# Kernel tuning notes

Hardware: AMD Instinct MI355X
Metric: run time of the kernel (lower is better)

The kernel has to match this reference:

```python
import jax, jax.numpy as jnp
import numpy as np

N, E, D_IN, D_H = 20000, 320000, 512, 512
ALPHA = 0.1
LAMBDA = 1.0

def setup_inputs() -> dict:
    key = jax.random.key(0)
    ks = jax.random.split(key, 12)
    feat = jax.random.normal(ks[0], (N, D_IN), dtype=jnp.float32)
    src = jax.random.randint(ks[1], (E,), 0, N, dtype=jnp.int32)
    dst = jax.random.randint(ks[2], (E,), 0, N, dtype=jnp.int32)
    s = 0.05
    fc_w = jax.random.normal(ks[3], (D_H, D_IN), dtype=jnp.float32) * s  # torch Linear: [out,in]
    fc_b = jax.random.normal(ks[4], (D_H,), dtype=jnp.float32) * s
    w1_1 = jax.random.normal(ks[5], (D_H, D_H), dtype=jnp.float32) * s
    w2_1 = jax.random.normal(ks[6], (D_H, D_H), dtype=jnp.float32) * s
    b_1 = jax.random.normal(ks[7], (D_H,), dtype=jnp.float32) * s
    w1_2 = jax.random.normal(ks[8], (D_H, D_H), dtype=jnp.float32) * s
    w2_2 = jax.random.normal(ks[9], (D_H, D_H), dtype=jnp.float32) * s
    b_2 = jax.random.normal(ks[10], (D_H,), dtype=jnp.float32) * s
    return {"feat": feat, "src": src, "dst": dst, "fc_w": fc_w, "fc_b": fc_b,
            "w1_1": w1_1, "w2_1": w2_1, "b_1": b_1,
            "w1_2": w1_2, "w2_2": w2_2, "b_2": b_2}


def _gcn2_layer(h, h0, src, dst, norm, w1, w2, b, layer):
    # DGL GCN2Conv (project_initial_features=False)
    beta = float(np.log(LAMBDA / layer + 1.0))
    x = h * norm                      # [N, D]
    agg = jax.ops.segment_sum(x[src], dst, num_segments=h.shape[0])  # SpMM: sum over in-neighbors
    agg = agg * norm
    f = agg * (1.0 - ALPHA)
    f0 = h0 * ALPHA
    rst = ((1.0 - beta) * f + beta * (f @ w1)
           + (1.0 - beta) * f0 + beta * (f0 @ w2) + b)
    return jax.nn.relu(rst)


def reference(feat, src, dst, fc_w, fc_b, w1_1, w2_1, b_1, w1_2, w2_2, b_2):
    n = feat.shape[0]
    h = feat @ fc_w.T + fc_b          # initial projection
    # symmetric norm from in-degrees (clamped at 1), as in DGL
    deg = jax.ops.segment_sum(jnp.ones_like(dst, dtype=h.dtype), dst, num_segments=n)
    norm = jnp.clip(deg, 1.0, None) ** -0.5
    norm = norm[:, None]
    res = _gcn2_layer(h, h, src, dst, norm, w1_1, w2_1, b_1, layer=1)
    out = _gcn2_layer(res, h, src, dst, norm, w1_2, w2_2, b_2, layer=2)
    return out
```

## Files before the change

kernel.cpp:

```cpp
#include <hip/hip_runtime.h>
#include <hip/hip_bf16.h>
#include <stdint.h>
#include <stddef.h>

typedef __bf16 bf16_t;
typedef __bf16 bf16x4 __attribute__((ext_vector_type(4)));
typedef __bf16 bf16x8 __attribute__((ext_vector_type(8)));
typedef float floatx4 __attribute__((ext_vector_type(4)));

#define NN 20000
#define EE 320000
#define DD 512
#define CAP 96
#define BETA1 0.6931471805599453f
#define BETA2 0.40546510810816444f

__device__ __forceinline__ void gload16(const bf16_t* g, bf16_t* l) {
  __builtin_amdgcn_global_load_lds((const __attribute__((address_space(1))) uint32_t*)g,
                                   (__attribute__((address_space(3))) uint32_t*)l, 16, 0, 0);
}

__global__ void bucket_kernel(const int* __restrict__ src, const int* __restrict__ dst,
                              int* __restrict__ cnt, int* __restrict__ esrc, int E) {
  int e = blockIdx.x * 256 + threadIdx.x;
  if (e < E) {
    int d = dst[e];
    int pos = atomicAdd(&cnt[d], 1);
    if (pos < CAP) esrc[d * CAP + pos] = src[e];
  }
}

__global__ void norm_kernel(const int* __restrict__ cnt, float* __restrict__ nrm, int n) {
  int i = blockIdx.x * 256 + threadIdx.x;
  if (i < n) nrm[i] = 1.0f / sqrtf(fmaxf((float)cnt[i], 1.0f));
}

__global__ void cvt_kernel(const float* __restrict__ in, bf16_t* __restrict__ out, int n4) {
  int i = blockIdx.x * 256 + threadIdx.x;
  if (i < n4) {
    float4 v = ((const float4*)in)[i];
    bf16x4 o = {(bf16_t)v.x, (bf16_t)v.y, (bf16_t)v.z, (bf16_t)v.w};
    ((bf16x4*)out)[i] = o;
  }
}

__global__ void transpose_cat(const float* __restrict__ W1, const float* __restrict__ W2,
                              bf16_t* __restrict__ BT, int K) {
  __shared__ bf16_t tile[32][33];
  int k0 = blockIdx.y * 32;
  int n0 = blockIdx.x * 32;
  int tx = threadIdx.x, ty = threadIdx.y;
  const float* W = (k0 < 512) ? W1 : W2;
  int kk = (k0 < 512) ? k0 : (k0 - 512);
#pragma unroll
  for (int i = 0; i < 32; i += 8)
    tile[ty + i][tx] = (bf16_t)W[(size_t)(kk + ty + i) * 512 + n0 + tx];
  __syncthreads();
#pragma unroll
  for (int i = 0; i < 32; i += 8)
    BT[(size_t)(n0 + ty + i) * K + k0 + tx] = tile[tx][ty + i];
}

__global__ __launch_bounds__(256) void aggregate_kernel(
    const bf16_t* __restrict__ hin, const float* __restrict__ nrm,
    const int* __restrict__ cnt, const int* __restrict__ esrc,
    bf16_t* __restrict__ Acat) {
  int node = blockIdx.x * 4 + (threadIdx.x >> 6);
  if (node >= NN) return;
  int lane = threadIdx.x & 63;
  const int* eb = esrc + (size_t)node * CAP;
  int n_e = cnt[node];
  n_e = n_e < CAP ? n_e : CAP;

  float acc[8] = {};
  bf16x8 v0 = {}, v1 = {}, v2 = {}, v3 = {}, v4 = {}, v5 = {}, v6 = {}, v7 = {};
  float ns0 = 0, ns1 = 0, ns2 = 0, ns3 = 0, ns4 = 0, ns5 = 0, ns6 = 0, ns7 = 0;

#define LOADJ(j, idx)                                                  \
  {                                                                    \
    int s = eb[idx];                                                   \
    ns##j = nrm[s];                                                    \
    v##j = *(const bf16x8*)(hin + (size_t)s * DD + lane * 8);          \
  }
#define SLOT(j, i)                                                     \
  if ((i) + (j) < n_e) {                                               \
    bf16x8 a = v##j; float na = ns##j;                                 \
    if ((i) + (j) + 8 < n_e) LOADJ(j, (i) + (j) + 8)                   \
    _Pragma("unroll")                                                  \
    for (int k = 0; k < 8; ++k) acc[k] += na * (float)a[k];            \
  }

  if (0 < n_e) LOADJ(0, 0)
  if (1 < n_e) LOADJ(1, 1)
  if (2 < n_e) LOADJ(2, 2)
  if (3 < n_e) LOADJ(3, 3)
  if (4 < n_e) LOADJ(4, 4)
  if (5 < n_e) LOADJ(5, 5)
  if (6 < n_e) LOADJ(6, 6)
  if (7 < n_e) LOADJ(7, 7)

  for (int i = 0; i < n_e; i += 8) {
    SLOT(0, i)
    SLOT(1, i)
    SLOT(2, i)
    SLOT(3, i)
    SLOT(4, i)
    SLOT(5, i)
    SLOT(6, i)
    SLOT(7, i)
  }
#undef SLOT
#undef LOADJ

  float nd = 0.9f * nrm[node];
  bf16x8 ob;
#pragma unroll
  for (int k = 0; k < 8; ++k) ob[k] = (bf16_t)(nd * acc[k]);
  *(bf16x8*)(Acat + (size_t)node * 1024 + lane * 8) = ob;
}

template <int MODE>
__global__ __launch_bounds__(256) void gemm_kernel(
    const bf16_t* __restrict__ A, const bf16_t* __restrict__ BT,
    int lda, int ldb, int K, int M,
    const float* __restrict__ bias,
    const bf16_t* __restrict__ acat_ro, float beta,
    float* __restrict__ outf, bf16_t* __restrict__ outb,
    bf16_t* __restrict__ acat2) {
  __shared__ bf16_t As[2][64 * 64];
  __shared__ bf16_t Bs[2][128 * 64];

  const int bid = blockIdx.x;
  const int mt = (bid >> 5) * 8 + (bid & 7);
  const int nt = (bid >> 3) & 3;
  const int m0 = mt * 64;
  if (m0 >= M) return;
  const int n0 = nt * 128;

  const int t = threadIdx.x;
  const int lane = t & 63;
  const int w = t >> 6;
  const int wm = w & 1, wn = w >> 1;
  const int quad = lane >> 4, m16 = lane & 15;

  const int tr = t >> 3;
  const int gc = (t & 7) ^ (tr & 7);
  int arow0 = m0 + tr;      arow0 = arow0 < M ? arow0 : M - 1;
  int arow1 = m0 + tr + 32; arow1 = arow1 < M ? arow1 : M - 1;
  const bf16_t* agp0 = A + (size_t)arow0 * lda + gc * 8;
  const bf16_t* agp1 = A + (size_t)arow1 * lda + gc * 8;
  const bf16_t* bgp0 = BT + (size_t)(n0 + tr) * ldb + gc * 8;
  const bf16_t* bgp1 = BT + (size_t)(n0 + tr + 32) * ldb + gc * 8;
  const bf16_t* bgp2 = BT + (size_t)(n0 + tr + 64) * ldb + gc * 8;
  const bf16_t* bgp3 = BT + (size_t)(n0 + tr + 96) * ldb + gc * 8;

#define STAGE(buf, ko)                              \
  gload16(agp0 + (ko), &As[buf][t * 8]);            \
  gload16(agp1 + (ko), &As[buf][(t + 256) * 8]);    \
  gload16(bgp0 + (ko), &Bs[buf][t * 8]);            \
  gload16(bgp1 + (ko), &Bs[buf][(t + 256) * 8]);    \
  gload16(bgp2 + (ko), &Bs[buf][(t + 512) * 8]);    \
  gload16(bgp3 + (ko), &Bs[buf][(t + 768) * 8]);

  floatx4 acc[2][4] = {};
  const int niter = K >> 6;

  STAGE(0, 0)

  for (int kt = 0; kt < niter; ++kt) {
    __syncthreads();
    const int b = kt & 1;
    if (kt + 1 < niter) {
      const int ko = (kt + 1) * 64;
      STAGE(b ^ 1, ko)
    }

#pragma unroll
    for (int ks = 0; ks < 2; ++ks) {
      bf16x8 af[2], bfr[4];
#pragma unroll
      for (int i = 0; i < 2; ++i) {
        int arow = wm * 32 + i * 16 + m16;
        int cc = (ks * 4 + quad) ^ (arow & 7);
        af[i] = *(const bf16x8*)(&As[b][(arow * 8 + cc) * 8]);
      }
#pragma unroll
      for (int j = 0; j < 4; ++j) {
        int brow = wn * 64 + j * 16 + m16;
        int cc = (ks * 4 + quad) ^ (brow & 7);
        bfr[j] = *(const bf16x8*)(&Bs[b][(brow * 8 + cc) * 8]);
      }
#pragma unroll
      for (int i = 0; i < 2; ++i)
#pragma unroll
        for (int j = 0; j < 4; ++j)
          acc[i][j] = __builtin_amdgcn_mfma_f32_16x16x32_bf16(af[i], bfr[j], acc[i][j], 0, 0, 0);
    }
  }
#undef STAGE

#pragma unroll
  for (int i = 0; i < 2; ++i) {
#pragma unroll
    for (int j = 0; j < 4; ++j) {
      int col = n0 + wn * 64 + j * 16 + m16;
      float bv = bias[col];
#pragma unroll
      for (int p = 0; p < 4; ++p) {
        int row = m0 + wm * 32 + i * 16 + quad * 4 + p;
        if (row < M) {
          size_t idx = (size_t)row * DD + col;
          float v = acc[i][j][p];
          if constexpr (MODE == 0) {
            float hv = v + bv;
            outb[idx] = (bf16_t)hv;
            acat2[(size_t)row * 1024 + 512 + col] = (bf16_t)(0.1f * hv);
          } else {
            float fsv = (float)acat_ro[(size_t)row * 1024 + col] +
                        (float)acat_ro[(size_t)row * 1024 + 512 + col];
            float r = (1.0f - beta) * fsv + beta * v + bv;
            r = fmaxf(r, 0.0f);
            if constexpr (MODE == 1) outb[idx] = (bf16_t)r;
            else outf[idx] = r;
          }
        }
      }
    }
  }
}

extern "C" void kernel_launch(void* const* d_in, const int* in_sizes, int n_in,
                              void* d_out, int out_size, void* d_ws, size_t ws_size,
                              hipStream_t stream) {
  const float* feat = (const float*)d_in[0];
  const int* src = (const int*)d_in[1];
  const int* dst = (const int*)d_in[2];
  const float* fc_w = (const float*)d_in[3];
  const float* fc_b = (const float*)d_in[4];
  const float* w1_1 = (const float*)d_in[5];
  const float* w2_1 = (const float*)d_in[6];
  const float* b_1  = (const float*)d_in[7];
  const float* w1_2 = (const float*)d_in[8];
  const float* w2_2 = (const float*)d_in[9];
  const float* b_2  = (const float*)d_in[10];
  float* out = (float*)d_out;

  char* ws = (char*)d_ws;
  size_t off = 0;
  auto alloc = [&](size_t bytes) {
    char* p = ws + off;
    off += (bytes + 255) & ~(size_t)255;
    return p;
  };
  const size_t NDf = (size_t)NN * DD;
  bf16_t* h_bf   = (bf16_t*)alloc(NDf * sizeof(bf16_t));
  bf16_t* res_bf = (bf16_t*)alloc(NDf * sizeof(bf16_t));
  bf16_t* featb  = (bf16_t*)alloc(NDf * sizeof(bf16_t));
  bf16_t* Acat   = (bf16_t*)alloc((size_t)NN * 1024 * sizeof(bf16_t));
  bf16_t* BW0    = (bf16_t*)alloc((size_t)512 * 512 * sizeof(bf16_t));
  bf16_t* BT1    = (bf16_t*)alloc((size_t)512 * 1024 * sizeof(bf16_t));
  bf16_t* BT2    = (bf16_t*)alloc((size_t)512 * 1024 * sizeof(bf16_t));
  int*    cnt    = (int*)alloc((size_t)NN * sizeof(int));
  float*  nrm    = (float*)alloc((size_t)NN * sizeof(float));
  int*    esrc   = (int*)alloc((size_t)NN * CAP * sizeof(int));

  hipMemsetAsync(cnt, 0, (size_t)NN * sizeof(int), stream);
  bucket_kernel<<<(EE + 255) / 256, 256, 0, stream>>>(src, dst, cnt, esrc, EE);
  norm_kernel<<<(NN + 255) / 256, 256, 0, stream>>>(cnt, nrm, NN);

  cvt_kernel<<<(int)(NDf / 4 / 256), 256, 0, stream>>>(feat, featb, (int)(NDf / 4));
  cvt_kernel<<<(512 * 512 / 4) / 256, 256, 0, stream>>>(fc_w, BW0, 512 * 512 / 4);

  transpose_cat<<<dim3(16, 32), dim3(32, 8), 0, stream>>>(w1_1, w2_1, BT1, 1024);
  transpose_cat<<<dim3(16, 32), dim3(32, 8), 0, stream>>>(w1_2, w2_2, BT2, 1024);

  const int gblocks = 1280;

  gemm_kernel<0><<<gblocks, 256, 0, stream>>>(featb, BW0, 512, 512, 512, NN, fc_b,
                                              nullptr, 0.0f, nullptr, h_bf, Acat);

  aggregate_kernel<<<(NN + 3) / 4, 256, 0, stream>>>(h_bf, nrm, cnt, esrc, Acat);
  gemm_kernel<1><<<gblocks, 256, 0, stream>>>(Acat, BT1, 1024, 1024, 1024, NN, b_1,
                                              Acat, BETA1, nullptr, res_bf, nullptr);

  aggregate_kernel<<<(NN + 3) / 4, 256, 0, stream>>>(res_bf, nrm, cnt, esrc, Acat);
  gemm_kernel<2><<<gblocks, 256, 0, stream>>>(Acat, BT2, 1024, 1024, 1024, NN, b_2,
                                              Acat, BETA2, out, nullptr, nullptr);
}
```

Measured before the change: 363.1 us.

## Triple-buffer GEMM LDS staging with explicit vmcnt waits

Moves the GEMM main loop from double to triple buffering in LDS. Tiles are prefetched two iterations ahead, and the loop waits with s_waitcnt vmcnt(6) so the newest stage's loads can stay in flight while the current tile is computed. The goal is to hide more global-load latency behind the MFMA work. In exchange, LDS per block grows from 48KB to 72KB, which may cut occupancy, and the hand-written waitcnt and barrier code depends on the exact count of outstanding loads to stay correct.

```diff
diff --git a/kernel.cpp b/kernel.cpp
--- a/kernel.cpp
+++ b/kernel.cpp
@@ -127,8 +127,8 @@
     const bf16_t* __restrict__ acat_ro, float beta,
     float* __restrict__ outf, bf16_t* __restrict__ outb,
     bf16_t* __restrict__ acat2) {
-  __shared__ bf16_t As[2][64 * 64];
-  __shared__ bf16_t Bs[2][128 * 64];
+  __shared__ bf16_t As[3][64 * 64];
+  __shared__ bf16_t Bs[3][128 * 64];
 
   const int bid = blockIdx.x;
   const int mt = (bid >> 5) * 8 + (bid & 7);
@@ -162,42 +162,58 @@
   gload16(bgp2 + (ko), &Bs[buf][(t + 512) * 8]);    \
   gload16(bgp3 + (ko), &Bs[buf][(t + 768) * 8]);
 
+#define COMPUTE(b)                                                               \
+  _Pragma("unroll")                                                              \
+  for (int ks = 0; ks < 2; ++ks) {                                               \
+    bf16x8 af[2], bfr[4];                                                        \
+    _Pragma("unroll")                                                            \
+    for (int i = 0; i < 2; ++i) {                                                \
+      int arow = wm * 32 + i * 16 + m16;                                         \
+      int cc = (ks * 4 + quad) ^ (arow & 7);                                     \
+      af[i] = *(const bf16x8*)(&As[b][(arow * 8 + cc) * 8]);                     \
+    }                                                                            \
+    _Pragma("unroll")                                                            \
+    for (int j = 0; j < 4; ++j) {                                                \
+      int brow = wn * 64 + j * 16 + m16;                                         \
+      int cc = (ks * 4 + quad) ^ (brow & 7);                                     \
+      bfr[j] = *(const bf16x8*)(&Bs[b][(brow * 8 + cc) * 8]);                    \
+    }                                                                            \
+    _Pragma("unroll")                                                            \
+    for (int i = 0; i < 2; ++i)                                                  \
+      _Pragma("unroll")                                                          \
+      for (int j = 0; j < 4; ++j)                                                \
+        acc[i][j] = __builtin_amdgcn_mfma_f32_16x16x32_bf16(af[i], bfr[j],       \
+                                                            acc[i][j], 0, 0, 0); \
+  }
+
   floatx4 acc[2][4] = {};
   const int niter = K >> 6;
 
   STAGE(0, 0)
-
-  for (int kt = 0; kt < niter; ++kt) {
-    __syncthreads();
-    const int b = kt & 1;
-    if (kt + 1 < niter) {
-      const int ko = (kt + 1) * 64;
-      STAGE(b ^ 1, ko)
+  STAGE(1, 64)
+
+  int cur = 0;
+  for (int kt = 0; kt < niter - 1; ++kt) {
+    asm volatile("s_waitcnt vmcnt(6)" ::: "memory");
+    asm volatile("s_waitcnt lgkmcnt(0)" ::: "memory");
+    __builtin_amdgcn_s_barrier();
+    __builtin_amdgcn_sched_barrier(0);
+    if (kt + 2 < niter) {
+      int nxt = cur + 2; nxt = nxt >= 3 ? nxt - 3 : nxt;
+      const int ko = (kt + 2) * 64;
+      STAGE(nxt, ko)
     }
-
-#pragma unroll
-    for (int ks = 0; ks < 2; ++ks) {
-      bf16x8 af[2], bfr[4];
-#pragma unroll
-      for (int i = 0; i < 2; ++i) {
-        int arow = wm * 32 + i * 16 + m16;
-        int cc = (ks * 4 + quad) ^ (arow & 7);
-        af[i] = *(const bf16x8*)(&As[b][(arow * 8 + cc) * 8]);
-      }
-#pragma unroll
-      for (int j = 0; j < 4; ++j) {
-        int brow = wn * 64 + j * 16 + m16;
-        int cc = (ks * 4 + quad) ^ (brow & 7);
-        bfr[j] = *(const bf16x8*)(&Bs[b][(brow * 8 + cc) * 8]);
-      }
-#pragma unroll
-      for (int i = 0; i < 2; ++i)
-#pragma unroll
-        for (int j = 0; j < 4; ++j)
-          acc[i][j] = __builtin_amdgcn_mfma_f32_16x16x32_bf16(af[i], bfr[j], acc[i][j], 0, 0, 0);
-    }
-  }
+    COMPUTE(cur)
+    cur = (cur == 2) ? 0 : cur + 1;
+  }
+  asm volatile("s_waitcnt vmcnt(0)" ::: "memory");
+  asm volatile("s_waitcnt lgkmcnt(0)" ::: "memory");
+  __builtin_amdgcn_s_barrier();
+  __builtin_amdgcn_sched_barrier(0);
+  COMPUTE(cur)
+
 #undef STAGE
+#undef COMPUTE
 
 #pragma unroll
   for (int i = 0; i < 2; ++i) {
```

After: 382.7 us. 1.05x slower.

## Pre-tile GEMM operands into MFMA fragment layout and drop LDS staging

Applied to the files above, without the earlier changes.

Operands (features, weights, and the aggregated Acat buffer) are now written in a blocked layout that matches the MFMA fragment order. This lets the GEMM load fragments straight from global memory with no LDS double buffering and no barriers. The conversion, transpose and count-zeroing kernels are merged into one prep kernel, and the norm kernel is removed by computing rsqrt of the degree inline in aggregation. The risk is that each wave reads its fragments from global memory independently, with no sharing through LDS across the block, so L2 traffic and latency exposure may rise.

```diff
diff --git a/kernel.cpp b/kernel.cpp
--- a/kernel.cpp
+++ b/kernel.cpp
@@ -12,16 +12,14 @@
 #define EE 320000
 #define DD 512
 #define CAP 96
+#define NBLK 313
 #define BETA1 0.6931471805599453f
 #define BETA2 0.40546510810816444f
 
-__device__ __forceinline__ void gload16(const bf16_t* g, bf16_t* l) {
-  __builtin_amdgcn_global_load_lds((const __attribute__((address_space(1))) uint32_t*)g,
-                                   (__attribute__((address_space(3))) uint32_t*)l, 16, 0, 0);
-}
-
-__global__ void bucket_kernel(const int* __restrict__ src, const int* __restrict__ dst,
-                              int* __restrict__ cnt, int* __restrict__ esrc, int E) {
+
+__global__ __launch_bounds__(256) void bucket_kernel(
+    const int* __restrict__ src, const int* __restrict__ dst,
+    int* __restrict__ cnt, int* __restrict__ esrc, int E) {
   int e = blockIdx.x * 256 + threadIdx.x;
   if (e < E) {
     int d = dst[e];
@@ -30,47 +28,64 @@
   }
 }
 
-__global__ void norm_kernel(const int* __restrict__ cnt, float* __restrict__ nrm, int n) {
-  int i = blockIdx.x * 256 + threadIdx.x;
-  if (i < n) nrm[i] = 1.0f / sqrtf(fmaxf((float)cnt[i], 1.0f));
-}
-
-__global__ void cvt_kernel(const float* __restrict__ in, bf16_t* __restrict__ out, int n4) {
-  int i = blockIdx.x * 256 + threadIdx.x;
-  if (i < n4) {
-    float4 v = ((const float4*)in)[i];
-    bf16x4 o = {(bf16_t)v.x, (bf16_t)v.y, (bf16_t)v.z, (bf16_t)v.w};
-    ((bf16x4*)out)[i] = o;
-  }
-}
-
-__global__ void transpose_cat(const float* __restrict__ W1, const float* __restrict__ W2,
-                              bf16_t* __restrict__ BT, int K) {
-  __shared__ bf16_t tile[32][33];
-  int k0 = blockIdx.y * 32;
-  int n0 = blockIdx.x * 32;
-  int tx = threadIdx.x, ty = threadIdx.y;
-  const float* W = (k0 < 512) ? W1 : W2;
-  int kk = (k0 < 512) ? k0 : (k0 - 512);
-#pragma unroll
-  for (int i = 0; i < 32; i += 8)
-    tile[ty + i][tx] = (bf16_t)W[(size_t)(kk + ty + i) * 512 + n0 + tx];
-  __syncthreads();
-#pragma unroll
-  for (int i = 0; i < 32; i += 8)
-    BT[(size_t)(n0 + ty + i) * K + k0 + tx] = tile[tx][ty + i];
+#define PREP_BLOCKS 5727
+__global__ __launch_bounds__(256) void prep_kernel(
+    const float* __restrict__ feat, const float* __restrict__ fc_w,
+    const float* __restrict__ w1_1, const float* __restrict__ w2_1,
+    const float* __restrict__ w1_2, const float* __restrict__ w2_2,
+    bf16_t* __restrict__ featb2, bf16_t* __restrict__ bw0,
+    bf16_t* __restrict__ bt1, bf16_t* __restrict__ bt2,
+    int* __restrict__ cnt) {
+  int b = blockIdx.x, t = threadIdx.x;
+  if (b < 5008) {
+    int c = b * 256 + t;
+    int kc = c & 63, r = (c >> 6) & 63, blk = c >> 12;
+    int row = blk * 64 + r;
+    if (row < NN) {
+      const float* s = feat + (size_t)row * 512 + kc * 8;
+      float4 v0 = *(const float4*)s, v1 = *(const float4*)(s + 4);
+      bf16x8 o = {(bf16_t)v0.x, (bf16_t)v0.y, (bf16_t)v0.z, (bf16_t)v0.w,
+                  (bf16_t)v1.x, (bf16_t)v1.y, (bf16_t)v1.z, (bf16_t)v1.w};
+      *(bf16x8*)(featb2 + ((size_t)(blk * 64 + kc) * 64 + r) * 8) = o;
+    }
+  } else if (b < 5136) {
+    int c = (b - 5008) * 256 + t;
+    int kc = c & 63, r = (c >> 6) & 63, blk = c >> 12;
+    const float* s = fc_w + (size_t)(blk * 64 + r) * 512 + kc * 8;
+    float4 v0 = *(const float4*)s, v1 = *(const float4*)(s + 4);
+    bf16x8 o = {(bf16_t)v0.x, (bf16_t)v0.y, (bf16_t)v0.z, (bf16_t)v0.w,
+                (bf16_t)v1.x, (bf16_t)v1.y, (bf16_t)v1.z, (bf16_t)v1.w};
+    *(bf16x8*)(bw0 + ((size_t)(blk * 64 + kc) * 64 + r) * 8) = o;
+  } else if (b < 5648) {
+    int base = (b < 5392) ? 5136 : 5392;
+    const float* Wa = (b < 5392) ? w1_1 : w1_2;
+    const float* Wb = (b < 5392) ? w2_1 : w2_2;
+    bf16_t* bt = (b < 5392) ? bt1 : bt2;
+    int c = (b - base) * 256 + t;
+    int nr = c & 63, kc = (c >> 6) & 127, nblk = c >> 13;
+    const float* W = (kc < 64) ? Wa : Wb;
+    int kcw = kc & 63;
+    int n = nblk * 64 + nr;
+    bf16x8 o;
+#pragma unroll
+    for (int e = 0; e < 8; ++e)
+      o[e] = (bf16_t)W[(size_t)(kcw * 8 + e) * 512 + n];
+    *(bf16x8*)(bt + (size_t)c * 8) = o;
+  } else {
+    int i = (b - 5648) * 256 + t;
+    if (i < NN) cnt[i] = 0;
+  }
 }
 
 __global__ __launch_bounds__(256) void aggregate_kernel(
-    const bf16_t* __restrict__ hin, const float* __restrict__ nrm,
-    const int* __restrict__ cnt, const int* __restrict__ esrc,
-    bf16_t* __restrict__ Acat) {
+    const bf16_t* __restrict__ hin, const int* __restrict__ cnt,
+    const int* __restrict__ esrc, bf16_t* __restrict__ Acat) {
   int node = blockIdx.x * 4 + (threadIdx.x >> 6);
   if (node >= NN) return;
   int lane = threadIdx.x & 63;
   const int* eb = esrc + (size_t)node * CAP;
-  int n_e = cnt[node];
-  n_e = n_e < CAP ? n_e : CAP;
+  int ne_raw = cnt[node];
+  int n_e = ne_raw < CAP ? ne_raw : CAP;
 
   float acc[8] = {};
   bf16x8 v0 = {}, v1 = {}, v2 = {}, v3 = {}, v4 = {}, v5 = {}, v6 = {}, v7 = {};
@@ -79,7 +94,7 @@
 #define LOADJ(j, idx)                                                  \
   {                                                                    \
     int s = eb[idx];                                                   \
-    ns##j = nrm[s];                                                    \
+    ns##j = rsqrtf(fmaxf((float)cnt[s], 1.0f));                        \
     v##j = *(const bf16x8*)(hin + (size_t)s * DD + lane * 8);          \
   }
 #define SLOT(j, i)                                                     \
@@ -112,24 +127,21 @@
 #undef SLOT
 #undef LOADJ
 
-  float nd = 0.9f * nrm[node];
+  float nd = 0.9f * rsqrtf(fmaxf((float)ne_raw, 1.0f));
   bf16x8 ob;
 #pragma unroll
   for (int k = 0; k < 8; ++k) ob[k] = (bf16_t)(nd * acc[k]);
-  *(bf16x8*)(Acat + (size_t)node * 1024 + lane * 8) = ob;
+  *(bf16x8*)(Acat + (((size_t)(node >> 6) * 128 + lane) * 64 + (node & 63)) * 8) = ob;
 }
 
 template <int MODE>
 __global__ __launch_bounds__(256) void gemm_kernel(
-    const bf16_t* __restrict__ A, const bf16_t* __restrict__ BT,
-    int lda, int ldb, int K, int M,
+    const bf16_t* __restrict__ A2, const bf16_t* __restrict__ B2,
+    int Kc, int M,
     const float* __restrict__ bias,
     const bf16_t* __restrict__ acat_ro, float beta,
     float* __restrict__ outf, bf16_t* __restrict__ outb,
     bf16_t* __restrict__ acat2) {
-  __shared__ bf16_t As[2][64 * 64];
-  __shared__ bf16_t Bs[2][128 * 64];
-
   const int bid = blockIdx.x;
   const int mt = (bid >> 5) * 8 + (bid & 7);
   const int nt = (bid >> 3) & 3;
@@ -143,61 +155,31 @@
   const int wm = w & 1, wn = w >> 1;
   const int quad = lane >> 4, m16 = lane & 15;
 
-  const int tr = t >> 3;
-  const int gc = (t & 7) ^ (tr & 7);
-  int arow0 = m0 + tr;      arow0 = arow0 < M ? arow0 : M - 1;
-  int arow1 = m0 + tr + 32; arow1 = arow1 < M ? arow1 : M - 1;
-  const bf16_t* agp0 = A + (size_t)arow0 * lda + gc * 8;
-  const bf16_t* agp1 = A + (size_t)arow1 * lda + gc * 8;
-  const bf16_t* bgp0 = BT + (size_t)(n0 + tr) * ldb + gc * 8;
-  const bf16_t* bgp1 = BT + (size_t)(n0 + tr + 32) * ldb + gc * 8;
-  const bf16_t* bgp2 = BT + (size_t)(n0 + tr + 64) * ldb + gc * 8;
-  const bf16_t* bgp3 = BT + (size_t)(n0 + tr + 96) * ldb + gc * 8;
-
-#define STAGE(buf, ko)                              \
-  gload16(agp0 + (ko), &As[buf][t * 8]);            \
-  gload16(agp1 + (ko), &As[buf][(t + 256) * 8]);    \
-  gload16(bgp0 + (ko), &Bs[buf][t * 8]);            \
-  gload16(bgp1 + (ko), &Bs[buf][(t + 256) * 8]);    \
-  gload16(bgp2 + (ko), &Bs[buf][(t + 512) * 8]);    \
-  gload16(bgp3 + (ko), &Bs[buf][(t + 768) * 8]);
+  const bf16_t* pa = A2 + (((size_t)mt * Kc + quad) * 64 + wm * 32 + m16) * 8;
+  const bf16_t* pb = B2 + (((size_t)(nt * 2 + wn) * Kc + quad) * 64 + m16) * 8;
 
   floatx4 acc[2][4] = {};
-  const int niter = K >> 6;
-
-  STAGE(0, 0)
-
+  const int niter = Kc >> 2;
+
+#pragma unroll 4
   for (int kt = 0; kt < niter; ++kt) {
-    __syncthreads();
-    const int b = kt & 1;
-    if (kt + 1 < niter) {
-      const int ko = (kt + 1) * 64;
-      STAGE(b ^ 1, ko)
-    }
-
-#pragma unroll
-    for (int ks = 0; ks < 2; ++ks) {
-      bf16x8 af[2], bfr[4];
-#pragma unroll
-      for (int i = 0; i < 2; ++i) {
-        int arow = wm * 32 + i * 16 + m16;
-        int cc = (ks * 4 + quad) ^ (arow & 7);
-        af[i] = *(const bf16x8*)(&As[b][(arow * 8 + cc) * 8]);
-      }
-#pragma unroll
-      for (int j = 0; j < 4; ++j) {
-        int brow = wn * 64 + j * 16 + m16;
-        int cc = (ks * 4 + quad) ^ (brow & 7);
-        bfr[j] = *(const bf16x8*)(&Bs[b][(brow * 8 + cc) * 8]);
-      }
-#pragma unroll
-      for (int i = 0; i < 2; ++i)
-#pragma unroll
-        for (int j = 0; j < 4; ++j)
-          acc[i][j] = __builtin_amdgcn_mfma_f32_16x16x32_bf16(af[i], bfr[j], acc[i][j], 0, 0, 0);
-    }
-  }
-#undef STAGE
+    bf16x8 af0 = *(const bf16x8*)(pa);
+    bf16x8 af1 = *(const bf16x8*)(pa + 128);
+    bf16x8 bf0 = *(const bf16x8*)(pb);
+    bf16x8 bf1 = *(const bf16x8*)(pb + 128);
+    bf16x8 bf2 = *(const bf16x8*)(pb + 256);
+    bf16x8 bf3 = *(const bf16x8*)(pb + 384);
+    acc[0][0] = __builtin_amdgcn_mfma_f32_16x16x32_bf16(af0, bf0, acc[0][0], 0, 0, 0);
+    acc[0][1] = __builtin_amdgcn_mfma_f32_16x16x32_bf16(af0, bf1, acc[0][1], 0, 0, 0);
+    acc[0][2] = __builtin_amdgcn_mfma_f32_16x16x32_bf16(af0, bf2, acc[0][2], 0, 0, 0);
+    acc[0][3] = __builtin_amdgcn_mfma_f32_16x16x32_bf16(af0, bf3, acc[0][3], 0, 0, 0);
+    acc[1][0] = __builtin_amdgcn_mfma_f32_16x16x32_bf16(af1, bf0, acc[1][0], 0, 0, 0);
+    acc[1][1] = __builtin_amdgcn_mfma_f32_16x16x32_bf16(af1, bf1, acc[1][1], 0, 0, 0);
+    acc[1][2] = __builtin_amdgcn_mfma_f32_16x16x32_bf16(af1, bf2, acc[1][2], 0, 0, 0);
+    acc[1][3] = __builtin_amdgcn_mfma_f32_16x16x32_bf16(af1, bf3, acc[1][3], 0, 0, 0);
+    pa += 2048;
+    pb += 2048;
+  }
 
 #pragma unroll
   for (int i = 0; i < 2; ++i) {
@@ -214,10 +196,13 @@
           if constexpr (MODE == 0) {
             float hv = v + bv;
             outb[idx] = (bf16_t)hv;
-            acat2[(size_t)row * 1024 + 512 + col] = (bf16_t)(0.1f * hv);
+            acat2[((size_t)(mt * 128 + 64 + (col >> 3)) * 64 + (row & 63)) * 8 +
+                  (col & 7)] = (bf16_t)(0.1f * hv);
           } else {
-            float fsv = (float)acat_ro[(size_t)row * 1024 + col] +
-                        (float)acat_ro[(size_t)row * 1024 + 512 + col];
+            size_t base = ((size_t)(mt * 128 + (col >> 3)) * 64 + (row & 63)) * 8 +
+                          (col & 7);
+            float fsv = (float)acat_ro[base] +
+                        (float)acat_ro[base + (size_t)64 * 64 * 8];
             float r = (1.0f - beta) * fsv + beta * v + bv;
             r = fmaxf(r, 0.0f);
             if constexpr (MODE == 1) outb[idx] = (bf16_t)r;
@@ -255,35 +240,28 @@
   const size_t NDf = (size_t)NN * DD;
   bf16_t* h_bf   = (bf16_t*)alloc(NDf * sizeof(bf16_t));
   bf16_t* res_bf = (bf16_t*)alloc(NDf * sizeof(bf16_t));
-  bf16_t* featb  = (bf16_t*)alloc(NDf * sizeof(bf16_t));
-  bf16_t* Acat   = (bf16_t*)alloc((size_t)NN * 1024 * sizeof(bf16_t));
-  bf16_t* BW0    = (bf16_t*)alloc((size_t)512 * 512 * sizeof(bf16_t));
-  bf16_t* BT1    = (bf16_t*)alloc((size_t)512 * 1024 * sizeof(bf16_t));
-  bf16_t* BT2    = (bf16_t*)alloc((size_t)512 * 1024 * sizeof(bf16_t));
+  bf16_t* featb2 = (bf16_t*)alloc((size_t)NBLK * 64 * 64 * 8 * sizeof(bf16_t));
+  bf16_t* Acat2  = (bf16_t*)alloc((size_t)NBLK * 128 * 64 * 8 * sizeof(bf16_t));
+  bf16_t* BW0b   = (bf16_t*)alloc((size_t)8 * 64 * 64 * 8 * sizeof(bf16_t));
+  bf16_t* BT1b   = (bf16_t*)alloc((size_t)8 * 128 * 64 * 8 * sizeof(bf16_t));
+  bf16_t* BT2b   = (bf16_t*)alloc((size_t)8 * 128 * 64 * 8 * sizeof(bf16_t));
   int*    cnt    = (int*)alloc((size_t)NN * sizeof(int));
-  float*  nrm    = (float*)alloc((size_t)NN * sizeof(float));
   int*    esrc   = (int*)alloc((size_t)NN * CAP * sizeof(int));
 
-  hipMemsetAsync(cnt, 0, (size_t)NN * sizeof(int), stream);
+  prep_kernel<<<PREP_BLOCKS, 256, 0, stream>>>(feat, fc_w, w1_1, w2_1, w1_2, w2_2,
+                                               featb2, BW0b, BT1b, BT2b, cnt);
   bucket_kernel<<<(EE + 255) / 256, 256, 0, stream>>>(src, dst, cnt, esrc, EE);
-  norm_kernel<<<(NN + 255) / 256, 256, 0, stream>>>(cnt, nrm, NN);
-
-  cvt_kernel<<<(int)(NDf / 4 / 256), 256, 0, stream>>>(feat, featb, (int)(NDf / 4));
-  cvt_kernel<<<(512 * 512 / 4) / 256, 256, 0, stream>>>(fc_w, BW0, 512 * 512 / 4);
-
-  transpose_cat<<<dim3(16, 32), dim3(32, 8), 0, stream>>>(w1_1, w2_1, BT1, 1024);
-  transpose_cat<<<dim3(16, 32), dim3(32, 8), 0, stream>>>(w1_2, w2_2, BT2, 1024);
 
   const int gblocks = 1280;
 
-  gemm_kernel<0><<<gblocks, 256, 0, stream>>>(featb, BW0, 512, 512, 512, NN, fc_b,
-                                              nullptr, 0.0f, nullptr, h_bf, Acat);
-
-  aggregate_kernel<<<(NN + 3) / 4, 256, 0, stream>>>(h_bf, nrm, cnt, esrc, Acat);
-  gemm_kernel<1><<<gblocks, 256, 0, stream>>>(Acat, BT1, 1024, 1024, 1024, NN, b_1,
-                                              Acat, BETA1, nullptr, res_bf, nullptr);
-
-  aggregate_kernel<<<(NN + 3) / 4, 256, 0, stream>>>(res_bf, nrm, cnt, esrc, Acat);
-  gemm_kernel<2><<<gblocks, 256, 0, stream>>>(Acat, BT2, 1024, 1024, 1024, NN, b_2,
-                                              Acat, BETA2, out, nullptr, nullptr);
-}
+  gemm_kernel<0><<<gblocks, 256, 0, stream>>>(featb2, BW0b, 64, NN, fc_b,
+                                              nullptr, 0.0f, nullptr, h_bf, Acat2);
+
+  aggregate_kernel<<<(NN + 3) / 4, 256, 0, stream>>>(h_bf, cnt, esrc, Acat2);
+  gemm_kernel<1><<<gblocks, 256, 0, stream>>>(Acat2, BT1b, 128, NN, b_1,
+                                              Acat2, BETA1, nullptr, res_bf, nullptr);
+
+  aggregate_kernel<<<(NN + 3) / 4, 256, 0, stream>>>(res_bf, cnt, esrc, Acat2);
+  gemm_kernel<2><<<gblocks, 256, 0, stream>>>(Acat2, BT2b, 128, NN, b_2,
+                                              Acat2, BETA2, out, nullptr, nullptr);
+}
```

After: 391.0 us. 7.7% more time.

## Fuse preprocessing kernels into one prep launch and fold norm into first GEMM

Applied to the files above, without the earlier changes.

Replaces the memset, two fp32-to-bf16 conversion kernels and two weight transpose kernels with a single prep kernel that dispatches work by block index. The degree-norm computation moves into extra blocks of the first GEMM launch. This cuts kernel launches and the gaps between them, which matter at this total runtime. The new transpose reads weights with a strided, uncoalesced pattern and no shared-memory tile, which may cost bandwidth on the small weight matrices.

```diff
diff --git a/kernel.cpp b/kernel.cpp
--- a/kernel.cpp
+++ b/kernel.cpp
@@ -20,8 +20,9 @@
                                    (__attribute__((address_space(3))) uint32_t*)l, 16, 0, 0);
 }
 
-__global__ void bucket_kernel(const int* __restrict__ src, const int* __restrict__ dst,
-                              int* __restrict__ cnt, int* __restrict__ esrc, int E) {
+__global__ __launch_bounds__(256) void bucket_kernel(
+    const int* __restrict__ src, const int* __restrict__ dst,
+    int* __restrict__ cnt, int* __restrict__ esrc, int E) {
   int e = blockIdx.x * 256 + threadIdx.x;
   if (e < E) {
     int d = dst[e];
@@ -30,35 +31,42 @@
   }
 }
 
-__global__ void norm_kernel(const int* __restrict__ cnt, float* __restrict__ nrm, int n) {
-  int i = blockIdx.x * 256 + threadIdx.x;
-  if (i < n) nrm[i] = 1.0f / sqrtf(fmaxf((float)cnt[i], 1.0f));
-}
-
-__global__ void cvt_kernel(const float* __restrict__ in, bf16_t* __restrict__ out, int n4) {
-  int i = blockIdx.x * 256 + threadIdx.x;
-  if (i < n4) {
-    float4 v = ((const float4*)in)[i];
-    bf16x4 o = {(bf16_t)v.x, (bf16_t)v.y, (bf16_t)v.z, (bf16_t)v.w};
-    ((bf16x4*)out)[i] = o;
-  }
-}
-
-__global__ void transpose_cat(const float* __restrict__ W1, const float* __restrict__ W2,
-                              bf16_t* __restrict__ BT, int K) {
-  __shared__ bf16_t tile[32][33];
-  int k0 = blockIdx.y * 32;
-  int n0 = blockIdx.x * 32;
-  int tx = threadIdx.x, ty = threadIdx.y;
-  const float* W = (k0 < 512) ? W1 : W2;
-  int kk = (k0 < 512) ? k0 : (k0 - 512);
-#pragma unroll
-  for (int i = 0; i < 32; i += 8)
-    tile[ty + i][tx] = (bf16_t)W[(size_t)(kk + ty + i) * 512 + n0 + tx];
-  __syncthreads();
-#pragma unroll
-  for (int i = 0; i < 32; i += 8)
-    BT[(size_t)(n0 + ty + i) * K + k0 + tx] = tile[tx][ty + i];
+#define PREP_BLOCKS 5719
+__global__ __launch_bounds__(256) void prep_kernel(
+    const float* __restrict__ feat, const float* __restrict__ fc_w,
+    const float* __restrict__ w1_1, const float* __restrict__ w2_1,
+    const float* __restrict__ w1_2, const float* __restrict__ w2_2,
+    bf16_t* __restrict__ featb, bf16_t* __restrict__ bw0,
+    bf16_t* __restrict__ bt1, bf16_t* __restrict__ bt2,
+    int* __restrict__ cnt) {
+  int b = blockIdx.x, t = threadIdx.x;
+  if (b < 5128) {
+    const float* in = (b < 5000) ? feat : fc_w;
+    bf16_t* out = (b < 5000) ? featb : bw0;
+    size_t c = (size_t)(b < 5000 ? b : b - 5000) * 256 + t;
+    const float* s = in + c * 8;
+    float4 v0 = *(const float4*)s, v1 = *(const float4*)(s + 4);
+    bf16x8 o = {(bf16_t)v0.x, (bf16_t)v0.y, (bf16_t)v0.z, (bf16_t)v0.w,
+                (bf16_t)v1.x, (bf16_t)v1.y, (bf16_t)v1.z, (bf16_t)v1.w};
+    *(bf16x8*)(out + c * 8) = o;
+  } else if (b < 5640) {
+    int base = (b < 5384) ? 5128 : 5384;
+    const float* Wa = (b < 5384) ? w1_1 : w1_2;
+    const float* Wb = (b < 5384) ? w2_1 : w2_2;
+    bf16_t* bt = (b < 5384) ? bt1 : bt2;
+    int c = (b - base) * 256 + t;
+    int n = c >> 7, kc = c & 127;
+    const float* W = (kc < 64) ? Wa : Wb;
+    int kcw = kc & 63;
+    bf16x8 o;
+#pragma unroll
+    for (int e = 0; e < 8; ++e)
+      o[e] = (bf16_t)W[(size_t)(kcw * 8 + e) * 512 + n];
+    *(bf16x8*)(bt + (size_t)n * 1024 + kc * 8) = o;
+  } else {
+    int i = (b - 5640) * 256 + t;
+    if (i < NN) cnt[i] = 0;
+  }
 }
 
 __global__ __launch_bounds__(256) void aggregate_kernel(
@@ -126,11 +134,19 @@
     const float* __restrict__ bias,
     const bf16_t* __restrict__ acat_ro, float beta,
     float* __restrict__ outf, bf16_t* __restrict__ outb,
-    bf16_t* __restrict__ acat2) {
+    bf16_t* __restrict__ acat2,
+    const int* __restrict__ cnt, float* __restrict__ nrm) {
   __shared__ bf16_t As[2][64 * 64];
   __shared__ bf16_t Bs[2][128 * 64];
 
   const int bid = blockIdx.x;
+  if constexpr (MODE == 0) {
+    if (bid >= 1280) {
+      int i = (bid - 1280) * 256 + threadIdx.x;
+      if (i < NN) nrm[i] = 1.0f / sqrtf(fmaxf((float)cnt[i], 1.0f));
+      return;
+    }
+  }
   const int mt = (bid >> 5) * 8 + (bid & 7);
   const int nt = (bid >> 3) & 3;
   const int m0 = mt * 64;
@@ -264,26 +280,21 @@
   float*  nrm    = (float*)alloc((size_t)NN * sizeof(float));
   int*    esrc   = (int*)alloc((size_t)NN * CAP * sizeof(int));
 
-  hipMemsetAsync(cnt, 0, (size_t)NN * sizeof(int), stream);
+  prep_kernel<<<PREP_BLOCKS, 256, 0, stream>>>(feat, fc_w, w1_1, w2_1, w1_2, w2_2,
+                                               featb, BW0, BT1, BT2, cnt);
   bucket_kernel<<<(EE + 255) / 256, 256, 0, stream>>>(src, dst, cnt, esrc, EE);
-  norm_kernel<<<(NN + 255) / 256, 256, 0, stream>>>(cnt, nrm, NN);
-
-  cvt_kernel<<<(int)(NDf / 4 / 256), 256, 0, stream>>>(feat, featb, (int)(NDf / 4));
-  cvt_kernel<<<(512 * 512 / 4) / 256, 256, 0, stream>>>(fc_w, BW0, 512 * 512 / 4);
-
-  transpose_cat<<<dim3(16, 32), dim3(32, 8), 0, stream>>>(w1_1, w2_1, BT1, 1024);
-  transpose_cat<<<dim3(16, 32), dim3(32, 8), 0, stream>>>(w1_2, w2_2, BT2, 1024);
-
-  const int gblocks = 1280;
-
-  gemm_kernel<0><<<gblocks, 256, 0, stream>>>(featb, BW0, 512, 512, 512, NN, fc_b,
-                                              nullptr, 0.0f, nullptr, h_bf, Acat);
+
+  gemm_kernel<0><<<1280 + 79, 256, 0, stream>>>(featb, BW0, 512, 512, 512, NN, fc_b,
+                                                nullptr, 0.0f, nullptr, h_bf, Acat,
+                                                cnt, nrm);
 
   aggregate_kernel<<<(NN + 3) / 4, 256, 0, stream>>>(h_bf, nrm, cnt, esrc, Acat);
-  gemm_kernel<1><<<gblocks, 256, 0, stream>>>(Acat, BT1, 1024, 1024, 1024, NN, b_1,
-                                              Acat, BETA1, nullptr, res_bf, nullptr);
+  gemm_kernel<1><<<1280, 256, 0, stream>>>(Acat, BT1, 1024, 1024, 1024, NN, b_1,
+                                           Acat, BETA1, nullptr, res_bf, nullptr,
+                                           nullptr, nullptr);
 
   aggregate_kernel<<<(NN + 3) / 4, 256, 0, stream>>>(res_bf, nrm, cnt, esrc, Acat);
-  gemm_kernel<2><<<gblocks, 256, 0, stream>>>(Acat, BT2, 1024, 1024, 1024, NN, b_2,
-                                              Acat, BETA2, out, nullptr, nullptr);
-}
+  gemm_kernel<2><<<1280, 256, 0, stream>>>(Acat, BT2, 1024, 1024, 1024, NN, b_2,
+                                           Acat, BETA2, out, nullptr, nullptr,
+                                           nullptr, nullptr);
+}
```

Measured after the change: 360.7 us. No clear change (-0.7%).
